# Kernel tuning notes

Hardware: AMD Instinct MI355X
Metric: run time of the kernel (lower is better)

The kernel has to match this reference:

```python
import jax, jax.numpy as jnp
import numpy as np

NUM_HEADS = 16
BLOCK_SIZE = 64


def setup_inputs() -> dict:
    key = jax.random.key(0)
    ks = jax.random.split(key, 4)
    B, S, D = 4, 8192, 1024
    x = jax.random.normal(ks[0], (B, S, D), dtype=jnp.float32)
    Wq = jax.random.normal(ks[1], (D, D), dtype=jnp.float32) * 0.02
    Wk = jax.random.normal(ks[2], (D, D), dtype=jnp.float32) * 0.02
    Wv = jax.random.normal(ks[3], (D, D), dtype=jnp.float32) * 0.02
    bq = jnp.zeros((D,), dtype=jnp.float32)
    bk = jnp.zeros((D,), dtype=jnp.float32)
    bv = jnp.zeros((D,), dtype=jnp.float32)
    return {"x": x, "Wq": Wq, "bq": bq, "Wk": Wk, "bk": bk, "Wv": Wv, "bv": bv}


def reference(x, Wq, bq, Wk, bk, Wv, bv):
    # Block-diagonal local self-attention: token i attends only to tokens in
    # its own block [i//bs*bs, (i//bs+1)*bs). Equivalent to the original dense
    # mask, but computed block-wise (never materializing the SxS score matrix).
    B, S, D = x.shape
    H, bs = NUM_HEADS, BLOCK_SIZE
    d = D // H
    nb = S // bs

    q = (x @ Wq + bq).reshape(B, nb, bs, H, d)
    k = (x @ Wk + bk).reshape(B, nb, bs, H, d)
    v = (x @ Wv + bv).reshape(B, nb, bs, H, d)

    scale = 1.0 / jnp.sqrt(jnp.asarray(d, dtype=x.dtype))
    # per-block scores: [B, nb, H, bs, bs]
    scores = jnp.einsum("bnihd,bnjhd->bnhij", q, k) * scale
    attn = jax.nn.softmax(scores, axis=-1)
    out = jnp.einsum("bnhij,bnjhd->bnihd", attn, v)  # [B, nb, bs, H, d]
    return out.reshape(B, S, D)
```

## Files before the change

### kernel.cpp

```cpp
#include <hip/hip_runtime.h>
#include <hip/hip_bf16.h>

typedef __attribute__((ext_vector_type(8))) short short8;
typedef __attribute__((ext_vector_type(4))) float f32x4;
typedef unsigned short u16;

#define M_TOK   32768
#define DIM     1024
#define NHEAD   16
#define HDIM    64
#define NBLK    128
#define NKT     32

__device__ __forceinline__ u16 f2b(float f) {
  union { float f; unsigned u; } v; v.f = f;
  unsigned r = (v.u + 0x7FFFu + ((v.u >> 16) & 1u)) >> 16;
  return (u16)r;
}

__global__ void cvt_x_kernel(const float* __restrict__ in, u16* __restrict__ out, int n8) {
  int i = blockIdx.x * 256 + threadIdx.x;
  if (i >= n8) return;
  const float4* p = (const float4*)in + (size_t)i * 2;
  float4 a = p[0], c = p[1];
  short8 o;
  o[0] = (short)f2b(a.x); o[1] = (short)f2b(a.y); o[2] = (short)f2b(a.z); o[3] = (short)f2b(a.w);
  o[4] = (short)f2b(c.x); o[5] = (short)f2b(c.y); o[6] = (short)f2b(c.z); o[7] = (short)f2b(c.w);
  *((short8*)out + i) = o;
}

__global__ void cvt_wT_kernel(const float* __restrict__ Wq, const float* __restrict__ Wk,
                              const float* __restrict__ Wv, u16* __restrict__ wT) {
  int t = blockIdx.x * 256 + threadIdx.x;
  int mat = t >> 17;
  int rem = t & 131071;
  int kg  = rem >> 10;
  int n   = rem & 1023;
  const float* W = (mat == 0) ? Wq : (mat == 1) ? Wk : Wv;
  short8 v;
  #pragma unroll
  for (int i = 0; i < 8; ++i) v[i] = (short)f2b(W[(size_t)(kg * 8 + i) * DIM + n]);
  *(short8*)(wT + ((size_t)mat << 20) + (size_t)n * DIM + kg * 8) = v;
}

__global__ __launch_bounds__(512, 2) void qkv_gemm_kernel(
    const u16* __restrict__ xb, const u16* __restrict__ wT,
    const float* __restrict__ bq, const float* __restrict__ bk, const float* __restrict__ bv,
    u16* __restrict__ qb, u16* __restrict__ kb, u16* __restrict__ vb)
{
  __shared__ u16 lds[3][256 * 64];

  const int tid  = threadIdx.x;
  const int lane = tid & 63;
  const int wid  = tid >> 6;

  const int orig = blockIdx.x;
  const int wg   = (orig & 7) * 192 + (orig >> 3);
  const int bm   = wg / 12;
  const int bn   = wg % 12;
  const int mat  = bn >> 2;
  const int col0 = (bn & 3) << 8;
  const int row0 = bm << 8;
  const u16* Wm = wT + ((size_t)mat << 20);
  const float* bias = (mat == 0) ? bq : (mat == 1) ? bk : bv;
  u16* outp = (mat == 0) ? qb : (mat == 1) ? kb : vb;

  const int wr = wid >> 2;
  const int wc = wid & 3;

  const int l    = (lane & 7) ^ ((lane >> 3) & 7);
  const int rl0  = wid * 8 + (lane >> 3);
  const u16* gsrc0 = (l < 4)
      ? xb + (size_t)(row0 + rl0) * DIM + l * 8
      : Wm + (size_t)(col0 + rl0) * DIM + (l - 4) * 8;

  int aoff[8], boff[4];
  #pragma unroll
  for (int mi = 0; mi < 8; ++mi) {
    int r = wr * 128 + mi * 16 + (lane & 15);
    aoff[mi] = r * 64 + (((lane >> 4) ^ (r & 7)) << 3);
  }
  #pragma unroll
  for (int ni = 0; ni < 4; ++ni) {
    int r = wc * 64 + ni * 16 + (lane & 15);
    boff[ni] = r * 64 + (((4 + (lane >> 4)) ^ (r & 7)) << 3);
  }

  f32x4 acc[8][4] = {};

  auto STAGE = [&](int kt, int bi) {
    const u16* s = gsrc0 + kt * 32;
    #pragma unroll
    for (int c = 0; c < 4; ++c) {
      __builtin_amdgcn_global_load_lds(
          (const __attribute__((address_space(1))) void*)(s + (size_t)c * 64 * DIM),
          (__attribute__((address_space(3))) void*)(&lds[bi][c * 4096 + wid * 512]),
          16, 0, 0);
    }
  };

  STAGE(0, 0);
  STAGE(1, 1);

  int cur = 0;
  for (int t = 0; t < NKT; ++t) {
    if (t + 1 < NKT) asm volatile("s_waitcnt vmcnt(4)" ::: "memory");
    else             asm volatile("s_waitcnt vmcnt(0)" ::: "memory");
    __builtin_amdgcn_s_barrier();
    if (t + 2 < NKT) {
      int nb = cur >= 1 ? cur - 1 : cur + 2;
      STAGE(t + 2, nb);
    }
    const u16* B = &lds[cur][0];
    short8 a[8], b[4];
    #pragma unroll
    for (int mi = 0; mi < 8; ++mi) a[mi] = *(const short8*)(B + aoff[mi]);
    #pragma unroll
    for (int ni = 0; ni < 4; ++ni) b[ni] = *(const short8*)(B + boff[ni]);
    __builtin_amdgcn_s_setprio(1);
    #pragma unroll
    for (int mi = 0; mi < 8; ++mi)
      #pragma unroll
      for (int ni = 0; ni < 4; ++ni)
        acc[mi][ni] = __builtin_amdgcn_mfma_f32_16x16x32_bf16(a[mi], b[ni], acc[mi][ni], 0, 0, 0);
    __builtin_amdgcn_s_setprio(0);
    cur = cur < 2 ? cur + 1 : 0;
  }

  #pragma unroll
  for (int ni = 0; ni < 4; ++ni) {
    int gcol = col0 + wc * 64 + ni * 16 + (lane & 15);
    float bb = bias[gcol];
    #pragma unroll
    for (int mi = 0; mi < 8; ++mi) {
      int grow = row0 + wr * 128 + mi * 16 + ((lane >> 4) << 2);
      #pragma unroll
      for (int r = 0; r < 4; ++r)
        outp[(size_t)(grow + r) * DIM + gcol] = f2b(acc[mi][ni][r] + bb);
    }
  }
}

__global__ __launch_bounds__(256) void blk_attn_kernel(
    const u16* __restrict__ qb, const u16* __restrict__ kb, const u16* __restrict__ vb,
    float* __restrict__ out)
{
  __shared__ u16 qs[64 * 72];
  __shared__ u16 ks[64 * 72];
  __shared__ u16 vts[64 * 72];
  __shared__ u16 ps[64 * 72];

  const int tid  = threadIdx.x;
  const int lane = tid & 63;
  const int wid  = tid >> 6;
  const int idx  = blockIdx.x;
  const int h    = idx & 15;
  const int blk  = (idx >> 4) & 127;
  const int b    = idx >> 11;
  const size_t s0 = (size_t)b * 8192 + (size_t)blk * 64;
  const int h0 = h * HDIM;

  {
    int i  = tid >> 2;
    int cg = (tid & 3) * 16;
    const u16* qg = qb + (s0 + i) * DIM + h0 + cg;
    *(short8*)(qs + i * 72 + cg)     = *(const short8*)qg;
    *(short8*)(qs + i * 72 + cg + 8) = *(const short8*)(qg + 8);
    const u16* kg = kb + (s0 + i) * DIM + h0 + cg;
    *(short8*)(ks + i * 72 + cg)     = *(const short8*)kg;
    *(short8*)(ks + i * 72 + cg + 8) = *(const short8*)(kg + 8);
    const u16* vg = vb + (s0 + i) * DIM + h0 + cg;
    short8 v0 = *(const short8*)vg;
    short8 v1 = *(const short8*)(vg + 8);
    #pragma unroll
    for (int e = 0; e < 8; ++e) {
      vts[(cg + e) * 72 + i]     = (u16)v0[e];
      vts[(cg + 8 + e) * 72 + i] = (u16)v1[e];
    }
  }
  __syncthreads();

  f32x4 S[4] = {};
  {
    short8 aq[2];
    #pragma unroll
    for (int kk = 0; kk < 2; ++kk)
      aq[kk] = *(const short8*)(qs + (wid * 16 + (lane & 15)) * 72 + kk * 32 + ((lane >> 4) << 3));
    #pragma unroll
    for (int jt = 0; jt < 4; ++jt)
      #pragma unroll
      for (int kk = 0; kk < 2; ++kk) {
        short8 bk_ = *(const short8*)(ks + (jt * 16 + (lane & 15)) * 72 + kk * 32 + ((lane >> 4) << 3));
        S[jt] = __builtin_amdgcn_mfma_f32_16x16x32_bf16(aq[kk], bk_, S[jt], 0, 0, 0);
      }
  }

  const float scale = 0.125f;
  float rinv[4];
  #pragma unroll
  for (int r = 0; r < 4; ++r) {
    float m = S[0][r] * scale;
    #pragma unroll
    for (int jt = 1; jt < 4; ++jt) m = fmaxf(m, S[jt][r] * scale);
    #pragma unroll
    for (int off = 1; off < 16; off <<= 1) m = fmaxf(m, __shfl_xor(m, off, 64));
    float s = 0.f;
    #pragma unroll
    for (int jt = 0; jt < 4; ++jt) {
      float e = __expf(S[jt][r] * scale - m);
      S[jt][r] = e;
      s += e;
    }
    #pragma unroll
    for (int off = 1; off < 16; off <<= 1) s += __shfl_xor(s, off, 64);
    rinv[r] = 1.0f / s;
  }

  #pragma unroll
  for (int jt = 0; jt < 4; ++jt)
    #pragma unroll
    for (int r = 0; r < 4; ++r)
      ps[(wid * 16 + ((lane >> 4) << 2) + r) * 72 + jt * 16 + (lane & 15)] = f2b(S[jt][r]);
  __syncthreads();

  f32x4 O[4] = {};
  {
    short8 pa[2];
    #pragma unroll
    for (int kk = 0; kk < 2; ++kk)
      pa[kk] = *(const short8*)(ps + (wid * 16 + (lane & 15)) * 72 + kk * 32 + ((lane >> 4) << 3));
    #pragma unroll
    for (int dt = 0; dt < 4; ++dt)
      #pragma unroll
      for (int kk = 0; kk < 2; ++kk) {
        short8 bv_ = *(const short8*)(vts + (dt * 16 + (lane & 15)) * 72 + kk * 32 + ((lane >> 4) << 3));
        O[dt] = __builtin_amdgcn_mfma_f32_16x16x32_bf16(pa[kk], bv_, O[dt], 0, 0, 0);
      }
  }

  #pragma unroll
  for (int dt = 0; dt < 4; ++dt)
    #pragma unroll
    for (int r = 0; r < 4; ++r)
      out[(s0 + wid * 16 + ((lane >> 4) << 2) + r) * DIM + h0 + dt * 16 + (lane & 15)] = O[dt][r] * rinv[r];
}

extern "C" void kernel_launch(void* const* d_in, const int* in_sizes, int n_in,
                              void* d_out, int out_size, void* d_ws, size_t ws_size,
                              hipStream_t stream) {
  const float* x  = (const float*)d_in[0];
  const float* Wq = (const float*)d_in[1];
  const float* bq = (const float*)d_in[2];
  const float* Wk = (const float*)d_in[3];
  const float* bk = (const float*)d_in[4];
  const float* Wv = (const float*)d_in[5];
  const float* bv = (const float*)d_in[6];
  float* out = (float*)d_out;

  char* ws = (char*)d_ws;
  u16* xb = (u16*)ws;
  u16* wT = (u16*)(ws + 67108864);
  u16* qb = (u16*)(ws + 73400320);
  u16* kb = (u16*)(ws + 140509184);
  u16* vb = (u16*)(ws + 207618048);

  cvt_x_kernel<<<16384, 256, 0, stream>>>(x, xb, 4194304);
  cvt_wT_kernel<<<1536, 256, 0, stream>>>(Wq, Wk, Wv, wT);
  qkv_gemm_kernel<<<1536, 512, 0, stream>>>(xb, wT, bq, bk, bv, qb, kb, vb);
  blk_attn_kernel<<<8192, 256, 0, stream>>>(qb, kb, vb, out);
}
```

Measured before the change: 362.7 us.

## Restructure QKV GEMM main loop into phased ping-pong schedule with 64-wide K tiles

Rewrites the QKV projection GEMM's main loop to use K tiles of 64 instead of 32, held in a two-buffer LDS layout (128 KB) split into A/B halves. Each K tile is processed in four barrier-separated phases that interleave LDS fragment loads, async global-to-LDS staging of upcoming sub-tiles, and prioritized MFMA bursts. The aim is to overlap memory traffic with matrix math more finely and halve the number of loop iterations. In exchange it adds many more barriers per iteration, uses more LDS per block (which may affect occupancy at two blocks per CU), and relies on delicate vmcnt/lgkmcnt accounting.

```diff
diff --git a/kernel.cpp b/kernel.cpp
--- a/kernel.cpp
+++ b/kernel.cpp
@@ -5,12 +5,11 @@
 typedef __attribute__((ext_vector_type(4))) float f32x4;
 typedef unsigned short u16;
 
-#define M_TOK   32768
 #define DIM     1024
 #define NHEAD   16
 #define HDIM    64
-#define NBLK    128
-#define NKT     32
+#define AS1 __attribute__((address_space(1)))
+#define AS3 __attribute__((address_space(3)))
 
 __device__ __forceinline__ u16 f2b(float f) {
   union { float f; unsigned u; } v; v.f = f;
@@ -43,12 +42,71 @@
   *(short8*)(wT + ((size_t)mat << 20) + (size_t)n * DIM + kg * 8) = v;
 }
 
+#define STAGE(matB, h, ktile) do { \
+  const u16* _s = (matB) ? srcB : srcA; \
+  _Pragma("unroll") \
+  for (int _j = 0; _j < 2; ++_j) { \
+    int _c = _j * 8 + wid; \
+    __builtin_amdgcn_global_load_lds( \
+      (const AS1 void*)(_s + (size_t)((h) * 128 + _c * 8) * DIM + (ktile) * 64), \
+      (AS3 void*)(lds + ((((ktile) & 1) << 15) + ((matB) << 14) + ((h) << 13) + _c * 512)), \
+      16, 0, 0); \
+  } \
+} while (0)
+
+#define LDA(d, g) do { \
+  _Pragma("unroll") \
+  for (int _mi = 0; _mi < 4; ++_mi) { \
+    int _r = abase + ((g) * 4 + _mi) * 1024 + ((d) << 15); \
+    a[_mi * 2]     = *(const short8*)(lds + _r + sx0); \
+    a[_mi * 2 + 1] = *(const short8*)(lds + _r + sx1); \
+  } \
+} while (0)
+
+#define LDB(d, dst, nB) do { \
+  _Pragma("unroll") \
+  for (int _ni = 0; _ni < 2; ++_ni) { \
+    int _r = bbase + ((nB) + _ni) * 1024 + ((d) << 15) + 16384; \
+    dst[_ni * 2]     = *(const short8*)(lds + _r + sx0); \
+    dst[_ni * 2 + 1] = *(const short8*)(lds + _r + sx1); \
+  } \
+} while (0)
+
+#define MF(g, nB, bset) do { \
+  _Pragma("unroll") \
+  for (int _mi = 0; _mi < 4; ++_mi) \
+    _Pragma("unroll") \
+    for (int _ni = 0; _ni < 2; ++_ni) \
+      _Pragma("unroll") \
+      for (int _kk = 0; _kk < 2; ++_kk) \
+        acc[(g) * 4 + _mi][(nB) + _ni] = __builtin_amdgcn_mfma_f32_16x16x32_bf16( \
+            a[_mi * 2 + _kk], bset[_ni * 2 + _kk], acc[(g) * 4 + _mi][(nB) + _ni], 0, 0, 0); \
+} while (0)
+
+#define PH_MID() do { \
+  __builtin_amdgcn_s_barrier(); \
+  asm volatile("s_waitcnt lgkmcnt(0)" ::: "memory"); \
+  __builtin_amdgcn_sched_barrier(0); \
+  __builtin_amdgcn_s_setprio(1); \
+} while (0)
+
+#define PH_END() do { \
+  __builtin_amdgcn_s_setprio(0); \
+  __builtin_amdgcn_s_barrier(); \
+} while (0)
+
+#define PH_END_VM(n) do { \
+  __builtin_amdgcn_s_setprio(0); \
+  asm volatile("s_waitcnt vmcnt(" #n ")" ::: "memory"); \
+  __builtin_amdgcn_s_barrier(); \
+} while (0)
+
 __global__ __launch_bounds__(512, 2) void qkv_gemm_kernel(
     const u16* __restrict__ xb, const u16* __restrict__ wT,
     const float* __restrict__ bq, const float* __restrict__ bk, const float* __restrict__ bv,
     u16* __restrict__ qb, u16* __restrict__ kb, u16* __restrict__ vb)
 {
-  __shared__ u16 lds[3][256 * 64];
+  __shared__ u16 lds[65536];
 
   const int tid  = threadIdx.x;
   const int lane = tid & 63;
@@ -67,73 +125,64 @@
 
   const int wr = wid >> 2;
   const int wc = wid & 3;
-
-  const int l    = (lane & 7) ^ ((lane >> 3) & 7);
-  const int rl0  = wid * 8 + (lane >> 3);
-  const u16* gsrc0 = (l < 4)
-      ? xb + (size_t)(row0 + rl0) * DIM + l * 8
-      : Wm + (size_t)(col0 + rl0) * DIM + (l - 4) * 8;
-
-  int aoff[8], boff[4];
-  #pragma unroll
-  for (int mi = 0; mi < 8; ++mi) {
-    int r = wr * 128 + mi * 16 + (lane & 15);
-    aoff[mi] = r * 64 + (((lane >> 4) ^ (r & 7)) << 3);
-  }
+  const int l15 = lane & 15, lhi = lane >> 4;
+
+  const int sr = lane >> 3;
+  const int sl = (lane & 7) ^ sr;
+  const u16* srcA = xb + (size_t)(row0 + sr) * DIM + sl * 8;
+  const u16* srcB = Wm + (size_t)(col0 + sr) * DIM + sl * 8;
+
+  const int sx0 = (lhi ^ (l15 & 7)) << 3;
+  const int sx1 = ((4 + lhi) ^ (l15 & 7)) << 3;
+  const int abase = (wr * 128 + l15) * 64;
+  const int bbase = (wc * 64 + l15) * 64;
+
+  f32x4 acc[8][4] = {};
+  short8 a[8], b01[4], b23[4];
+
+  STAGE(0, 0, 0); STAGE(0, 1, 0); STAGE(1, 0, 0); STAGE(1, 1, 0);
+  STAGE(0, 0, 1); STAGE(0, 1, 1);
+  asm volatile("s_waitcnt vmcnt(4)" ::: "memory");
+  __builtin_amdgcn_s_barrier();
+
+  #pragma unroll 1
+  for (int t = 0; t < 8; ++t) {
+    const int kt = 2 * t;
+    const bool pf = (t < 7);
+    LDA(0, 0); LDB(0, b01, 0);
+    STAGE(1, 0, kt + 1);
+    asm volatile("s_waitcnt lgkmcnt(8)" ::: "memory");
+    PH_MID(); MF(0, 0, b01); PH_END();
+    LDB(0, b23, 2);
+    STAGE(1, 1, kt + 1);
+    PH_MID(); MF(0, 2, b23); PH_END();
+    LDA(0, 1);
+    PH_MID(); MF(1, 2, b23); PH_END();
+    if (pf) STAGE(0, 0, kt + 2);
+    PH_MID(); MF(1, 0, b01);
+    if (pf) { PH_END_VM(2); } else { PH_END_VM(0); }
+    LDA(1, 0); LDB(1, b01, 0);
+    if (pf) STAGE(0, 1, kt + 2);
+    asm volatile("s_waitcnt lgkmcnt(8)" ::: "memory");
+    PH_MID(); MF(0, 0, b01); PH_END();
+    LDB(1, b23, 2);
+    if (pf) STAGE(1, 0, kt + 2);
+    PH_MID(); MF(0, 2, b23); PH_END();
+    LDA(1, 1);
+    if (pf) STAGE(1, 1, kt + 2);
+    PH_MID(); MF(1, 2, b23); PH_END();
+    if (pf) { STAGE(0, 0, kt + 3); STAGE(0, 1, kt + 3); }
+    PH_MID(); MF(1, 0, b01);
+    if (pf) { PH_END_VM(4); } else { PH_END_VM(0); }
+  }
+
   #pragma unroll
   for (int ni = 0; ni < 4; ++ni) {
-    int r = wc * 64 + ni * 16 + (lane & 15);
-    boff[ni] = r * 64 + (((4 + (lane >> 4)) ^ (r & 7)) << 3);
-  }
-
-  f32x4 acc[8][4] = {};
-
-  auto STAGE = [&](int kt, int bi) {
-    const u16* s = gsrc0 + kt * 32;
-    #pragma unroll
-    for (int c = 0; c < 4; ++c) {
-      __builtin_amdgcn_global_load_lds(
-          (const __attribute__((address_space(1))) void*)(s + (size_t)c * 64 * DIM),
-          (__attribute__((address_space(3))) void*)(&lds[bi][c * 4096 + wid * 512]),
-          16, 0, 0);
-    }
-  };
-
-  STAGE(0, 0);
-  STAGE(1, 1);
-
-  int cur = 0;
-  for (int t = 0; t < NKT; ++t) {
-    if (t + 1 < NKT) asm volatile("s_waitcnt vmcnt(4)" ::: "memory");
-    else             asm volatile("s_waitcnt vmcnt(0)" ::: "memory");
-    __builtin_amdgcn_s_barrier();
-    if (t + 2 < NKT) {
-      int nb = cur >= 1 ? cur - 1 : cur + 2;
-      STAGE(t + 2, nb);
-    }
-    const u16* B = &lds[cur][0];
-    short8 a[8], b[4];
-    #pragma unroll
-    for (int mi = 0; mi < 8; ++mi) a[mi] = *(const short8*)(B + aoff[mi]);
-    #pragma unroll
-    for (int ni = 0; ni < 4; ++ni) b[ni] = *(const short8*)(B + boff[ni]);
-    __builtin_amdgcn_s_setprio(1);
-    #pragma unroll
-    for (int mi = 0; mi < 8; ++mi)
-      #pragma unroll
-      for (int ni = 0; ni < 4; ++ni)
-        acc[mi][ni] = __builtin_amdgcn_mfma_f32_16x16x32_bf16(a[mi], b[ni], acc[mi][ni], 0, 0, 0);
-    __builtin_amdgcn_s_setprio(0);
-    cur = cur < 2 ? cur + 1 : 0;
-  }
-
-  #pragma unroll
-  for (int ni = 0; ni < 4; ++ni) {
-    int gcol = col0 + wc * 64 + ni * 16 + (lane & 15);
+    int gcol = col0 + wc * 64 + ni * 16 + l15;
     float bb = bias[gcol];
     #pragma unroll
     for (int mi = 0; mi < 8; ++mi) {
-      int grow = row0 + wr * 128 + mi * 16 + ((lane >> 4) << 2);
+      int grow = row0 + wr * 128 + mi * 16 + (lhi << 2);
       #pragma unroll
       for (int r = 0; r < 4; ++r)
         outp[(size_t)(grow + r) * DIM + gcol] = f2b(acc[mi][ni][r] + bb);
```

Measured after the change: 345.0 us. 1.05x faster.
